# Kernel optimization log

Measured on AMD Instinct MI355X. Metric: run time of the kernel, lower is better.

## Reference

```python
import jax, jax.numpy as jnp
import numpy as np

DIM = 768
NUM_HEADS = 12
HEAD_DIM = DIM // NUM_HEADS
SCALE = HEAD_DIM ** -0.5


def setup_inputs() -> dict:
    key = jax.random.key(0)
    k_x, k_qw, k_qb, k_pw, k_pb = jax.random.split(key, 5)
    B, N = 4, 2048
    x = jax.random.normal(k_x, (B, N, DIM), dtype=jnp.float32)
    s = 1.0 / np.sqrt(DIM)
    qkv_w = jax.random.normal(k_qw, (3 * DIM, DIM), dtype=jnp.float32) * s
    qkv_b = jax.random.normal(k_qb, (3 * DIM,), dtype=jnp.float32) * 0.02
    proj_w = jax.random.normal(k_pw, (DIM, DIM), dtype=jnp.float32) * s
    proj_b = jax.random.normal(k_pb, (DIM,), dtype=jnp.float32) * 0.02
    return {"x": x, "qkv_w": qkv_w, "qkv_b": qkv_b, "proj_w": proj_w, "proj_b": proj_b}


def reference(x, qkv_w, qkv_b, proj_w, proj_b):
    B, N, D = x.shape
    H, Hd = NUM_HEADS, HEAD_DIM
    # qkv linear: [B,N,3D] -> [3,B,H,N,Hd]
    qkv = (x @ qkv_w.T + qkv_b).reshape(B, N, 3, H, Hd).transpose(2, 0, 3, 1, 4)
    q, k, v = qkv[0], qkv[1], qkv[2]
    scores = jnp.einsum("bhnd,bhmd->bhnm", q, k) * SCALE  # [B,H,N,N]
    attn = jax.nn.softmax(scores, axis=-1)
    out = jnp.einsum("bhnm,bhmd->bhnd", attn, v)  # [B,H,N,Hd]
    out = out.transpose(0, 2, 1, 3).reshape(B, N, D)
    return out @ proj_w.T + proj_b
```

## Files before the change

### kernel.cpp

```cpp
#include <hip/hip_runtime.h>

#define SEQ 2048
#define NB 4
#define NH 12
#define DHEAD 64
#define DMODEL 768
#define D3 2304
#define MTOT 8192
#define QSCALE 0.18033688011112042f

typedef float f4v __attribute__((ext_vector_type(4)));
typedef float fl4 __attribute__((ext_vector_type(4)));
typedef short s8v __attribute__((ext_vector_type(8)));
typedef __bf16 b8v __attribute__((ext_vector_type(8)));
typedef unsigned int ui4 __attribute__((ext_vector_type(4)));
typedef unsigned int ui2 __attribute__((ext_vector_type(2)));
typedef unsigned short us4 __attribute__((ext_vector_type(4)));

#define GLDS16(g, l)                                                            \
  __builtin_amdgcn_global_load_lds(                                             \
      (const __attribute__((address_space(1))) void*)(g),                       \
      (__attribute__((address_space(3))) void*)(l), 16, 0, 0)

__device__ inline float fast_exp2(float x) {
#if __has_builtin(__builtin_amdgcn_exp2f)
  return __builtin_amdgcn_exp2f(x);
#else
  float r;
  asm("v_exp_f32 %0, %1" : "=v"(r) : "v"(x));
  return r;
#endif
}

template <typename T>
__device__ inline auto mfma_try(T a, T b, f4v c, int)
    -> decltype(__builtin_amdgcn_mfma_f32_16x16x32_bf16(a, b, c, 0, 0, 0)) {
  return __builtin_amdgcn_mfma_f32_16x16x32_bf16(a, b, c, 0, 0, 0);
}
template <typename T>
__device__ inline f4v mfma_try(T a, T b, f4v c, long) {
  return __builtin_amdgcn_mfma_f32_16x16x32_bf16(
      __builtin_bit_cast(b8v, a), __builtin_bit_cast(b8v, b), c, 0, 0, 0);
}
__device__ inline f4v mfma16(s8v a, s8v b, f4v c) { return mfma_try(a, b, c, 0); }

__device__ inline unsigned short f2bf(float f) {
  union { float f; unsigned u; } v; v.f = f;
  unsigned r = v.u + 0x7FFFu + ((v.u >> 16) & 1u);
  return (unsigned short)(r >> 16);
}

__device__ inline unsigned pack2(float a, float b) {
  unsigned ua = __builtin_bit_cast(unsigned, a) + 0x8000u;
  unsigned ub = __builtin_bit_cast(unsigned, b) + 0x8000u;
  return __builtin_amdgcn_perm(ub, ua, 0x07060302u);
}

#define NX4 1572864
#define NW14 442368
#define NW24 147456
__global__ void k_cvt(const float* __restrict__ x, const float* __restrict__ w1,
                      const float* __restrict__ w2, unsigned short* __restrict__ ox,
                      unsigned short* __restrict__ o1, unsigned short* __restrict__ o2) {
  int i = blockIdx.x * 256 + threadIdx.x;
  const float* src;
  unsigned short* dst;
  int off;
  if (i < NX4) { src = x; dst = ox; off = i; }
  else if (i < NX4 + NW14) { src = w1; dst = o1; off = i - NX4; }
  else if (i < NX4 + NW14 + NW24) { src = w2; dst = o2; off = i - NX4 - NW14; }
  else return;
  fl4 f = ((const fl4*)src)[off];
  us4 o;
  o[0] = f2bf(f[0]); o[1] = f2bf(f[1]); o[2] = f2bf(f[2]); o[3] = f2bf(f[3]);
  ((us4*)dst)[off] = o;
}

template <int EPI>
__global__ __launch_bounds__(256, 3) void k_gemm_nt(
    const unsigned short* __restrict__ A,
    const unsigned short* __restrict__ Bm,
    const float* __restrict__ bias,
    float* __restrict__ outF,
    unsigned short* __restrict__ outQ,
    unsigned short* __restrict__ outK,
    unsigned short* __restrict__ outV,
    int K) {
  __shared__ unsigned short As[128 * 64];
  __shared__ unsigned short Bs[128 * 64];
  const int tid = threadIdx.x;
  const int lane = tid & 63;
  const int wave = tid >> 6;
  const int wr = wave >> 1, wc = wave & 1;
  const int lr = lane & 15;
  const int lq = lane >> 4;
  const int rowBase = blockIdx.y * 128;
  const int colBase = blockIdx.x * 128;

  f4v acc[4][4];
#pragma unroll
  for (int i = 0; i < 4; ++i)
#pragma unroll
    for (int j = 0; j < 4; ++j) acc[i][j] = f4v{0.f, 0.f, 0.f, 0.f};

  const int srow = wave * 8 + (lane >> 3);
  const int scol = ((lane & 7) ^ ((lane >> 3) & 7)) * 8;
  const unsigned short* Ag0 = A + (long)(rowBase + srow) * K + scol;
  const unsigned short* Bg0 = Bm + (long)(colBase + srow) * K + scol;
  unsigned short* Al0 = &As[srow * 64 + (lane & 7) * 8];
  unsigned short* Bl0 = &Bs[srow * 64 + (lane & 7) * 8];
  const int kTiles = K >> 6;
  const int swz = (lr & 7);

  for (int kt = 0; kt < kTiles; ++kt) {
#pragma unroll
    for (int p = 0; p < 4; ++p) {
      GLDS16(Ag0 + kt * 64 + p * 32 * K, Al0 + p * 32 * 64);
      GLDS16(Bg0 + kt * 64 + p * 32 * K, Bl0 + p * 32 * 64);
    }
    __syncthreads();
#pragma unroll
    for (int ks = 0; ks < 2; ++ks) {
      s8v af[4], bf[4];
#pragma unroll
      for (int i = 0; i < 4; ++i)
        af[i] = *(const s8v*)&As[(wr * 64 + i * 16 + lr) * 64 + ((ks * 4 + lq) ^ swz) * 8];
#pragma unroll
      for (int j = 0; j < 4; ++j)
        bf[j] = *(const s8v*)&Bs[(wc * 64 + j * 16 + lr) * 64 + ((ks * 4 + lq) ^ swz) * 8];
#pragma unroll
      for (int i = 0; i < 4; ++i)
#pragma unroll
        for (int j = 0; j < 4; ++j) acc[i][j] = mfma16(af[i], bf[j], acc[i][j]);
    }
    __syncthreads();
  }

#pragma unroll
  for (int j = 0; j < 4; ++j) {
    const int col = colBase + wc * 64 + j * 16 + lr;
    const float bv = bias[col];
    if (EPI == 1) {
#pragma unroll
      for (int i = 0; i < 4; ++i)
#pragma unroll
        for (int e = 0; e < 4; ++e) {
          const int row = rowBase + wr * 64 + i * 16 + lq * 4 + e;
          outF[row * DMODEL + col] = acc[i][j][e] + bv;
        }
    } else {
      const int t = col / DMODEL;
      const int h = (col >> 6) % NH;
      const int hd = col & 63;
#pragma unroll
      for (int i = 0; i < 4; ++i) {
        const int row = rowBase + wr * 64 + i * 16 + lq * 4;
        const int b = row >> 11;
        const int n = row & 2047;
        if (t == 2) {
          const int bq = (n >> 2) & 7;
          const int np = (n & ~31) + ((bq & 3) << 3) + ((bq >> 2) << 2);
          float v0 = acc[i][j][0] + bv, v1 = acc[i][j][1] + bv;
          float v2 = acc[i][j][2] + bv, v3 = acc[i][j][3] + bv;
          *(ui2*)&outV[(((b * NH + h) * DHEAD) + hd) * SEQ + np] =
              ui2{pack2(v0, v1), pack2(v2, v3)};
        } else {
#pragma unroll
          for (int e = 0; e < 4; ++e) {
            const float v = acc[i][j][e] + bv;
            if (t == 0)
              outQ[(((b * NH + h) * SEQ) + n + e) * DHEAD + hd] = f2bf(v * QSCALE);
            else
              outK[(((b * NH + h) * SEQ) + n + e) * DHEAD + hd] = f2bf(v);
          }
        }
      }
    }
  }
}

__global__ __launch_bounds__(256, 3) void k_attn(
    const unsigned short* __restrict__ Q,
    const unsigned short* __restrict__ Kg,
    const unsigned short* __restrict__ Vt,
    unsigned short* __restrict__ Ob) {
  __shared__ unsigned short Ks[128 * 64];
  __shared__ unsigned short Vs[64 * 128];
  const int tid = threadIdx.x;
  const int lane = tid & 63;
  const int wave = tid >> 6;
  const int lr = lane & 15;
  const int lq = lane >> 4;
  const int bh = blockIdx.y;
  const int b = bh / NH, h = bh % NH;
  const int q0 = blockIdx.x * 128;
  const unsigned short* Qb = Q + (long)bh * SEQ * DHEAD;
  const unsigned short* Kb = Kg + (long)bh * SEQ * DHEAD;
  const unsigned short* Vb = Vt + (long)bh * DHEAD * SEQ;

  s8v qf[2][2];
#pragma unroll
  for (int i = 0; i < 2; ++i)
#pragma unroll
    for (int ss = 0; ss < 2; ++ss)
      qf[i][ss] = *(const s8v*)(Qb + (q0 + wave * 32 + i * 16 + lr) * DHEAD + ss * 32 + lq * 8);

  f4v o[2][4];
  f4v la[2] = {f4v{0.f, 0.f, 0.f, 0.f}, f4v{0.f, 0.f, 0.f, 0.f}};
  const f4v zc = f4v{0.f, 0.f, 0.f, 0.f};
  const s8v ones = {0x3F80, 0x3F80, 0x3F80, 0x3F80, 0x3F80, 0x3F80, 0x3F80, 0x3F80};
#pragma unroll
  for (int i = 0; i < 2; ++i)
#pragma unroll
    for (int jo = 0; jo < 4; ++jo) o[i][jo] = f4v{0.f, 0.f, 0.f, 0.f};

  const int srow = wave * 8 + (lane >> 3);
  const int scol = ((lane & 7) ^ ((lane >> 3) & 7)) * 8;
  const unsigned short* Kg0 = Kb + (long)srow * DHEAD + scol;
  unsigned short* Kl0 = &Ks[srow * 64 + (lane & 7) * 8];
  const int swz = (lr & 7);
  const int vdrow = wave * 4 + (lane >> 4);
  const int vchunk = (lane & 15) ^ vdrow;
  const unsigned short* Vg0 = Vb + (long)vdrow * SEQ + vchunk * 8;
  unsigned short* Vl0 = &Vs[vdrow * 128 + (lane & 15) * 8];

  for (int kt = 0; kt < SEQ / 128; ++kt) {
#pragma unroll
    for (int p = 0; p < 4; ++p)
      GLDS16(Kg0 + (long)(kt * 128 + p * 32) * DHEAD, Kl0 + p * 32 * 64);
#pragma unroll
    for (int p = 0; p < 4; ++p)
      GLDS16(Vg0 + (long)(p * 16) * SEQ + kt * 128, Vl0 + p * 16 * 128);
    __syncthreads();

    f4v s[2][8];
#pragma unroll
    for (int t = 0; t < 8; ++t) {
      s8v kf0 = *(const s8v*)&Ks[(t * 16 + lr) * 64 + ((0 * 4 + lq) ^ swz) * 8];
      s8v kf1 = *(const s8v*)&Ks[(t * 16 + lr) * 64 + ((1 * 4 + lq) ^ swz) * 8];
      s[0][t] = mfma16(kf0, qf[0][0], zc);
      s[1][t] = mfma16(kf0, qf[1][0], zc);
      s[0][t] = mfma16(kf1, qf[0][1], s[0][t]);
      s[1][t] = mfma16(kf1, qf[1][1], s[1][t]);
    }

    unsigned pk[2][8][2];
#pragma unroll
    for (int i = 0; i < 2; ++i)
#pragma unroll
      for (int t = 0; t < 8; ++t) {
        float p0 = fast_exp2(s[i][t][0]);
        float p1 = fast_exp2(s[i][t][1]);
        float p2 = fast_exp2(s[i][t][2]);
        float p3 = fast_exp2(s[i][t][3]);
        pk[i][t][0] = pack2(p0, p1);
        pk[i][t][1] = pack2(p2, p3);
      }

#pragma unroll
    for (int ss = 0; ss < 4; ++ss) {
      s8v vf[4];
#pragma unroll
      for (int jo = 0; jo < 4; ++jo)
        vf[jo] = *(const s8v*)&Vs[(jo * 16 + lr) * 128 + ((ss * 4 + lq) ^ lr) * 8];
#pragma unroll
      for (int i = 0; i < 2; ++i) {
        s8v pf = __builtin_bit_cast(
            s8v, ui4{pk[i][2 * ss][0], pk[i][2 * ss][1], pk[i][2 * ss + 1][0], pk[i][2 * ss + 1][1]});
        la[i] = mfma16(ones, pf, la[i]);
#pragma unroll
        for (int jo = 0; jo < 4; ++jo) o[i][jo] = mfma16(vf[jo], pf, o[i][jo]);
      }
    }
    __syncthreads();
  }

  float linv[2];
  linv[0] = 1.0f / la[0][0];
  linv[1] = 1.0f / la[1][0];

#pragma unroll
  for (int i = 0; i < 2; ++i) {
    const long nrow = (long)(b * SEQ + q0 + wave * 32 + i * 16 + lr) * DMODEL;
#pragma unroll
    for (int jo = 0; jo < 4; ++jo) {
      float v0 = o[i][jo][0] * linv[i];
      float v1 = o[i][jo][1] * linv[i];
      float v2 = o[i][jo][2] * linv[i];
      float v3 = o[i][jo][3] * linv[i];
      *(ui2*)(Ob + nrow + h * DHEAD + jo * 16 + lq * 4) = ui2{pack2(v0, v1), pack2(v2, v3)};
    }
  }
}

extern "C" void kernel_launch(void* const* d_in, const int* in_sizes, int n_in,
                              void* d_out, int out_size, void* d_ws, size_t ws_size,
                              hipStream_t stream) {
  (void)in_sizes; (void)n_in; (void)out_size; (void)ws_size;
  const float* x = (const float*)d_in[0];
  const float* qkv_w = (const float*)d_in[1];
  const float* qkv_b = (const float*)d_in[2];
  const float* proj_w = (const float*)d_in[3];
  const float* proj_b = (const float*)d_in[4];
  float* out = (float*)d_out;

  unsigned short* ws = (unsigned short*)d_ws;
  unsigned short* xb = ws;
  unsigned short* wqkvb = xb + 6291456;
  unsigned short* wprjb = wqkvb + 1769472;
  unsigned short* qb = wprjb + 589824;
  unsigned short* kb = qb + 6291456;
  unsigned short* vtb = kb + 6291456;
  unsigned short* aob = vtb + 6291456;

  k_cvt<<<(NX4 + NW14 + NW24 + 255) / 256, 256, 0, stream>>>(
      x, qkv_w, proj_w, xb, wqkvb, wprjb);

  k_gemm_nt<0><<<dim3(D3 / 128, MTOT / 128), 256, 0, stream>>>(
      xb, wqkvb, qkv_b, nullptr, qb, kb, vtb, DMODEL);
  k_attn<<<dim3(SEQ / 128, NB * NH), 256, 0, stream>>>(qb, kb, vtb, aob);
  k_gemm_nt<1><<<dim3(DMODEL / 128, MTOT / 128), 256, 0, stream>>>(
      aob, wprjb, proj_b, out, nullptr, nullptr, nullptr, DMODEL);
}
```

Baseline: 208.8 us.

## Swap GEMM operand roles so epilogue stores are contiguous vectors

The Q/K projection and the output projection now run as transposed GEMMs, with the weight matrix as the A operand and the activations as B. Each lane then holds four consecutive output features and can write packed bf16x4 or float4 stores instead of scattered scalar stores. The V projection is split into its own launch that keeps the original orientation and its transposed, permuted store. This adds an extra kernel launch and changes the block-to-tile mapping, which may affect cache reuse of the operands.

Result: no change. 207.1 us (-0.8%).

```diff
diff --git a/kernel.cpp b/kernel.cpp
--- a/kernel.cpp
+++ b/kernel.cpp
@@ -136,44 +136,48 @@
     __syncthreads();
   }
 
-#pragma unroll
-  for (int j = 0; j < 4; ++j) {
-    const int col = colBase + wc * 64 + j * 16 + lr;
-    const float bv = bias[col];
-    if (EPI == 1) {
-#pragma unroll
-      for (int i = 0; i < 4; ++i)
-#pragma unroll
-        for (int e = 0; e < 4; ++e) {
-          const int row = rowBase + wr * 64 + i * 16 + lq * 4 + e;
-          outF[row * DMODEL + col] = acc[i][j][e] + bv;
+  if (EPI == 0 || EPI == 1) {
+    const int fw = rowBase + wr * 64;
+    fl4 bv[4];
+#pragma unroll
+    for (int i = 0; i < 4; ++i) bv[i] = *(const fl4*)&bias[fw + i * 16 + lq * 4];
+    const int isQ = (EPI == 0) && (fw < DMODEL);
+    const int h = (fw >> 6) % NH;
+    const unsigned short* outQK = isQ ? outQ : outK;
+    const float scl = isQ ? QSCALE : 1.0f;
+#pragma unroll
+    for (int j = 0; j < 4; ++j) {
+      const int ng = colBase + wc * 64 + j * 16 + lr;
+#pragma unroll
+      for (int i = 0; i < 4; ++i) {
+        float v0 = acc[i][j][0] + bv[i][0], v1 = acc[i][j][1] + bv[i][1];
+        float v2 = acc[i][j][2] + bv[i][2], v3 = acc[i][j][3] + bv[i][3];
+        if (EPI == 1) {
+          *(fl4*)&outF[(long)ng * DMODEL + fw + i * 16 + lq * 4] = fl4{v0, v1, v2, v3};
+        } else {
+          const int b = ng >> 11, nn = ng & 2047;
+          unsigned short* dst = (unsigned short*)outQK +
+              (long)(((b * NH + h) * SEQ) + nn) * DHEAD + (i * 16 + lq * 4);
+          *(ui2*)dst = ui2{pack2(v0 * scl, v1 * scl), pack2(v2 * scl, v3 * scl)};
         }
-    } else {
-      const int t = col / DMODEL;
-      const int h = (col >> 6) % NH;
-      const int hd = col & 63;
+      }
+    }
+  } else {
+#pragma unroll
+    for (int j = 0; j < 4; ++j) {
+      const int col = colBase + wc * 64 + j * 16 + lr;
+      const float bvs = bias[col];
+      const int h = col >> 6, hd = col & 63;
 #pragma unroll
       for (int i = 0; i < 4; ++i) {
         const int row = rowBase + wr * 64 + i * 16 + lq * 4;
-        const int b = row >> 11;
-        const int n = row & 2047;
-        if (t == 2) {
-          const int bq = (n >> 2) & 7;
-          const int np = (n & ~31) + ((bq & 3) << 3) + ((bq >> 2) << 2);
-          float v0 = acc[i][j][0] + bv, v1 = acc[i][j][1] + bv;
-          float v2 = acc[i][j][2] + bv, v3 = acc[i][j][3] + bv;
-          *(ui2*)&outV[(((b * NH + h) * DHEAD) + hd) * SEQ + np] =
-              ui2{pack2(v0, v1), pack2(v2, v3)};
-        } else {
-#pragma unroll
-          for (int e = 0; e < 4; ++e) {
-            const float v = acc[i][j][e] + bv;
-            if (t == 0)
-              outQ[(((b * NH + h) * SEQ) + n + e) * DHEAD + hd] = f2bf(v * QSCALE);
-            else
-              outK[(((b * NH + h) * SEQ) + n + e) * DHEAD + hd] = f2bf(v);
-          }
-        }
+        const int b = row >> 11, n = row & 2047;
+        const int bq = (n >> 2) & 7;
+        const int np = (n & ~31) + ((bq & 3) << 3) + ((bq >> 2) << 2);
+        float v0 = acc[i][j][0] + bvs, v1 = acc[i][j][1] + bvs;
+        float v2 = acc[i][j][2] + bvs, v3 = acc[i][j][3] + bvs;
+        *(ui2*)&outV[(long)(((b * NH + h) * DHEAD) + hd) * SEQ + np] =
+            ui2{pack2(v0, v1), pack2(v2, v3)};
       }
     }
   }
@@ -316,9 +320,12 @@
   k_cvt<<<(NX4 + NW14 + NW24 + 255) / 256, 256, 0, stream>>>(
       x, qkv_w, proj_w, xb, wqkvb, wprjb);
 
-  k_gemm_nt<0><<<dim3(D3 / 128, MTOT / 128), 256, 0, stream>>>(
-      xb, wqkvb, qkv_b, nullptr, qb, kb, vtb, DMODEL);
+  k_gemm_nt<0><<<dim3(MTOT / 128, 2 * DMODEL / 128), 256, 0, stream>>>(
+      wqkvb, xb, qkv_b, nullptr, qb, kb, nullptr, DMODEL);
+  k_gemm_nt<2><<<dim3(DMODEL / 128, MTOT / 128), 256, 0, stream>>>(
+      xb, wqkvb + 2 * DMODEL * DMODEL, qkv_b + 2 * DMODEL, nullptr, nullptr, nullptr, vtb,
+      DMODEL);
   k_attn<<<dim3(SEQ / 128, NB * NH), 256, 0, stream>>>(qb, kb, vtb, aob);
-  k_gemm_nt<1><<<dim3(DMODEL / 128, MTOT / 128), 256, 0, stream>>>(
-      aob, wprjb, proj_b, out, nullptr, nullptr, nullptr, DMODEL);
-}
+  k_gemm_nt<1><<<dim3(MTOT / 128, DMODEL / 128), 256, 0, stream>>>(
+      wprjb, aob, proj_b, out, nullptr, nullptr, nullptr, DMODEL);
+}
```
